# Performance work log

Hardware: AMD Instinct MI355X
Metric: run time of the kernel (lower is better)

Reference implementation:

```python
import jax, jax.numpy as jnp
import numpy as np
from jax import lax

C = 64   # channels
R = 2    # SKM expansion ratio
M = 4    # number of dilated convs
EPS = 1e-6


def conv3_dilated(x, w, b, d):
    # 3x3 conv, dilation d, padding d (same spatial size)
    y = lax.conv_general_dilated(x, w, (1, 1), [(d, d), (d, d)],
                                 rhs_dilation=(d, d),
                                 dimension_numbers=('NCHW', 'OIHW', 'NCHW'))
    return y + b[None, :, None, None]


def ln2d(x, g, b):
    # LayerNorm over channel dim at each spatial position (NAFNet LayerNorm2d)
    mu = x.mean(1, keepdims=True)
    var = x.var(1, keepdims=True)
    return (x - mu) / jnp.sqrt(var + EPS) * g[None, :, None, None] + b[None, :, None, None]


def skm(x, dw, db, c1w, c1b, pw):
    # dw: [M,C,C,3,3], db: [M,C], c1w: [R*C,C], c1b: [R*C], pw: [R*C, M*C]
    D = jnp.stack([conv3_dilated(x, dw[i], db[i], 2 * (i + 1)) for i in range(M)])  # [M,B,C,H,W]
    Z = D.sum(0).mean((-2, -1))                      # [B,C] global avg pool of summed branches
    S = jax.nn.relu(Z @ c1w.T + c1b)                 # [B,R*C]
    Sw = jax.nn.softmax((S @ pw).reshape(-1, M, C), axis=-1)  # [B,M,C], softmax over C
    return jnp.einsum('mbchw,bmc->bchw', D, Sw)      # weighted sum of branches


def setup_inputs() -> dict:
    key = jax.random.key(0)
    ks = jax.random.split(key, 24)
    B, H, W = 4, 96, 256
    sc = 0.05
    inp = {
        'x_l': jax.random.normal(ks[0], (B, C, H, W), jnp.float32),
        'x_r': jax.random.normal(ks[1], (B, C, H, W), jnp.float32),
        'lnl_g': jnp.ones((C,), jnp.float32),
        'lnl_b': jnp.zeros((C,), jnp.float32),
        'lnr_g': jnp.ones((C,), jnp.float32),
        'lnr_b': jnp.zeros((C,), jnp.float32),
        'l_dw': jax.random.normal(ks[2], (M, C, C, 3, 3), jnp.float32) * sc,
        'l_db': jax.random.normal(ks[3], (M, C), jnp.float32) * sc,
        'l_c1w': jax.random.normal(ks[4], (R * C, C), jnp.float32) * sc,
        'l_c1b': jax.random.normal(ks[5], (R * C,), jnp.float32) * sc,
        'l_pw': jax.random.normal(ks[6], (R * C, M * C), jnp.float32) * sc,
        'r_dw': jax.random.normal(ks[7], (M, C, C, 3, 3), jnp.float32) * sc,
        'r_db': jax.random.normal(ks[8], (M, C), jnp.float32) * sc,
        'r_c1w': jax.random.normal(ks[9], (R * C, C), jnp.float32) * sc,
        'r_c1b': jax.random.normal(ks[10], (R * C,), jnp.float32) * sc,
        'r_pw': jax.random.normal(ks[11], (R * C, M * C), jnp.float32) * sc,
        'l2w': jax.random.normal(ks[12], (C, C), jnp.float32) * sc,
        'l2b': jax.random.normal(ks[13], (C,), jnp.float32) * sc,
        'r2w': jax.random.normal(ks[14], (C, C), jnp.float32) * sc,
        'r2b': jax.random.normal(ks[15], (C,), jnp.float32) * sc,
        'beta': jax.random.normal(ks[16], (1, C, 1, 1), jnp.float32) * sc,
        'gamma': jax.random.normal(ks[17], (1, C, 1, 1), jnp.float32) * sc,
    }
    return inp


def reference(x_l, x_r, lnl_g, lnl_b, lnr_g, lnr_b,
              l_dw, l_db, l_c1w, l_c1b, l_pw,
              r_dw, r_db, r_c1w, r_c1b, r_pw,
              l2w, l2b, r2w, r2b, beta, gamma):
    scale = C ** (-0.5)
    Ql = skm(ln2d(x_l, lnl_g, lnl_b), l_dw, l_db, l_c1w, l_c1b, l_pw).transpose(0, 2, 3, 1)  # [B,H,W,C]
    Qr = skm(ln2d(x_r, lnr_g, lnr_b), r_dw, r_db, r_c1w, r_c1b, r_pw).transpose(0, 2, 3, 1)  # [B,H,W,C]
    Vl = (jnp.einsum('bchw,dc->bdhw', x_l, l2w) + l2b[None, :, None, None]).transpose(0, 2, 3, 1)
    Vr = (jnp.einsum('bchw,dc->bdhw', x_r, r2w) + r2b[None, :, None, None]).transpose(0, 2, 3, 1)
    attn = jnp.einsum('bhwc,bhvc->bhwv', Ql, Qr) * scale  # shared score matrix [B,H,W,W]
    F_r2l = jnp.einsum('bhwv,bhvc->bhwc', jax.nn.softmax(attn, axis=-1), Vr).transpose(0, 3, 1, 2)
    F_l2r = jnp.einsum('bhwv,bhwc->bhvc', jax.nn.softmax(attn, axis=-2), Vl).transpose(0, 3, 1, 2)
    return x_l + F_r2l * beta, x_r + F_l2r * gamma
```

## Files before the change

### kernel.cpp

```cpp
#include <hip/hip_runtime.h>
#include <hip/hip_bf16.h>
#include <cstdint>

constexpr int NB = 4;
constexpr int NC = 64;
constexpr int NH = 96;
constexpr int NW = 256;
constexpr int HWp = NH * NW;
constexpr float EPS = 1e-6f;

typedef __attribute__((ext_vector_type(8))) short short8;
typedef __attribute__((ext_vector_type(4))) short short4t;
typedef __attribute__((ext_vector_type(4))) float f32x4;

static __device__ __forceinline__ short f2bf(float f) {
    __hip_bfloat16 h = __float2bfloat16(f);
    return *reinterpret_cast<short*>(&h);
}

__global__ __launch_bounds__(256) void k_lnv(const float* __restrict__ x_l,
                                             const float* __restrict__ x_r,
                                             const float* __restrict__ gl,
                                             const float* __restrict__ bl,
                                             const float* __restrict__ gr,
                                             const float* __restrict__ br,
                                             short* __restrict__ XBl,
                                             short* __restrict__ XBr,
                                             float* __restrict__ R,
                                             const float* __restrict__ w2l,
                                             const float* __restrict__ b2l,
                                             const float* __restrict__ w2r,
                                             const float* __restrict__ b2r,
                                             short* __restrict__ VL,
                                             short* __restrict__ VR) {
    __shared__ float smem[8704];
    const int h = blockIdx.y, sideb = blockIdx.z;
    const int side = sideb >> 2, b = sideb & 3;
    const int t = threadIdx.x;

    if (blockIdx.x == 4) {
        const float* x = side ? x_r : x_l;
        const float* g = side ? gr : gl;
        const float* bta = side ? br : bl;
        short* XB = side ? XBr : XBl;
        float* xm = smem;

        const float* xp = x + ((size_t)b * NC * NH + h) * NW + t;
        float v[64];
        float s = 0.f, sq = 0.f;
#pragma unroll
        for (int c = 0; c < 64; ++c) {
            float tv = xp[(size_t)c * HWp];
            v[c] = tv; s += tv; sq += tv * tv;
        }
        float mu = s * (1.f / 64.f);
        float var = sq * (1.f / 64.f) - mu * mu;
        float rs = rsqrtf(var + EPS);
#pragma unroll
        for (int c = 0; c < 64; ++c) v[c] = (v[c] - mu) * rs * g[c] + bta[c];

#pragma unroll
        for (int chunk = 0; chunk < 4; ++chunk) {
            short8 s0, s1;
#pragma unroll
            for (int j = 0; j < 8; ++j) {
                s0[j] = f2bf(v[chunk * 16 + j]);
                s1[j] = f2bf(v[chunk * 16 + 8 + j]);
            }
            short* xb = XB + (((size_t)(b * 4 + chunk) * NH + h) * NW + t) * 16;
            *(short8*)xb = s0;
            *(short8*)(xb + 8) = s1;
        }

#pragma unroll
        for (int p = 0; p < 2; ++p) {
            const int cbase = p * 32;
            __syncthreads();
#pragma unroll
            for (int c = 0; c < 32; ++c)
                xm[c * 256 + (((t >> 2) ^ (c & 7)) << 2) + (t & 3)] = v[cbase + c];
            __syncthreads();
            const int cc = t & 31, q = t >> 5;
            float rsum = 0.f;
            float4 fs0 = {0,0,0,0}, fs1 = {0,0,0,0}, ls0 = {0,0,0,0}, ls1 = {0,0,0,0};
#pragma unroll
            for (int i = 0; i < 8; ++i) {
                int j4 = q * 8 + i;
                float4 f = *(const float4*)&xm[cc * 256 + ((j4 ^ (cc & 7)) << 2)];
                rsum += (f.x + f.y) + (f.z + f.w);
                if (i == 0) fs0 = f;
                if (i == 1) fs1 = f;
                if (i == 6) ls0 = f;
                if (i == 7) ls1 = f;
            }
            __syncthreads();
            xm[cc * 8 + q] = rsum;
            if (q == 7) {
                *(float4*)&xm[256 + cc * 8] = ls0;
                *(float4*)&xm[256 + cc * 8 + 4] = ls1;
            }
            __syncthreads();
            if (t < 32) {
                const int c = t;
                float full = 0.f;
#pragma unroll
                for (int q2 = 0; q2 < 8; ++q2) full += xm[c * 8 + q2];
                float h0 = xm[256 + c * 8 + 0], h1 = xm[256 + c * 8 + 1];
                float h2 = xm[256 + c * 8 + 2], h3 = xm[256 + c * 8 + 3];
                float h4 = xm[256 + c * 8 + 4], h5 = xm[256 + c * 8 + 5];
                float h6 = xm[256 + c * 8 + 6], h7 = xm[256 + c * 8 + 7];
                float e2 = fs0.x + fs0.y;
                float e4 = e2 + fs0.z + fs0.w;
                float e6 = e4 + fs1.x + fs1.y;
                float e8 = e6 + fs1.z + fs1.w;
                float r2 = h6 + h7;
                float r4 = (h4 + h5) + r2;
                float r6 = r4 + (h2 + h3);
                float r8 = r6 + (h0 + h1);
                float* Rp = R + ((size_t)(sideb * 64 + cbase + c) * NH + h) * 9;
                Rp[0] = full; Rp[1] = e2; Rp[2] = e4; Rp[3] = e6; Rp[4] = e8;
                Rp[5] = r2;  Rp[6] = r4; Rp[7] = r6; Rp[8] = r8;
            }
        }
    } else {
        const int wt = blockIdx.x;
        const float* x  = side ? x_r : x_l;
        const float* w2 = side ? w2r : w2l;
        const float* b2 = side ? b2r : b2l;
        short* VT = side ? VR : VL;
        const int lane = t & 63, q = t >> 6;
        float* xs  = smem;
        float* w2t = smem + 4352;
        int w0 = wt * 64;
        const float* src = x + (size_t)(b * 64) * HWp + h * NW + w0;
        for (int idx = t; idx < 4096; idx += 256) {
            int ci = idx >> 6, col = idx & 63;
            xs[ci * 68 + col] = src[(size_t)ci * HWp + col];
        }
        for (int idx = t; idx < 4096; idx += 256) {
            int co = idx >> 6, ci = idx & 63;
            w2t[ci * 68 + co] = w2[co * 64 + ci];
        }
        __syncthreads();

        const int pl0 = (lane & 15) * 4;
        const int c0 = q * 16 + (lane >> 4) * 4;
        f32x4 a4[4];
#pragma unroll
        for (int cc = 0; cc < 4; ++cc) {
            float bb = b2[c0 + cc];
            a4[cc] = (f32x4){bb, bb, bb, bb};
        }
        for (int ci = 0; ci < 64; ++ci) {
            f32x4 xv = *(const f32x4*)(xs + ci * 68 + pl0);
            f32x4 wv = *(const f32x4*)(w2t + ci * 68 + c0);
            a4[0] += xv * wv[0];
            a4[1] += xv * wv[1];
            a4[2] += xv * wv[2];
            a4[3] += xv * wv[3];
        }
        __syncthreads();
#pragma unroll
        for (int cc = 0; cc < 4; ++cc)
            *(f32x4*)(xs + (c0 + cc) * 68 + pl0) = a4[cc];
        __syncthreads();
        {
            int s = t & 63, g2 = t >> 6;
            int u = (s >> 2) + 16 * (s & 3);
#pragma unroll
            for (int cc = 0; cc < 16; ++cc) {
                int ch = g2 * 16 + cc;
                VT[((size_t)(b * 64 + ch) * NH + h) * NW + w0 + s] = f2bf(xs[ch * 68 + u]);
            }
        }
    }
}

__global__ __launch_bounds__(128) void k_comb(const float* __restrict__ R,
                                              float* __restrict__ T) {
    int x = blockIdx.x;
    int side = x >> 8, rem = x & 255, b = rem >> 6, ci = rem & 63;
    __shared__ float rp[NH][9];
    int t = threadIdx.x;
    const float* src = R + (size_t)x * NH * 9;
    for (int i = t; i < NH * 9; i += 128) ((float*)rp)[i] = src[i];
    __syncthreads();
    if (t < 36) {
        int m = t / 9, kh = (t % 9) / 3, kw = t % 3;
        int d = 2 * (m + 1);
        int r0 = (kh == 2) ? d : 0;
        int r1 = (kh == 0) ? NH - d : NH;
        float s = 0.f;
        for (int r = r0; r < r1; ++r) {
            float rowv = rp[r][0];
            if (kw == 0) rowv -= rp[r][5 + m];
            else if (kw == 2) rowv -= rp[r][1 + m];
            s += rowv;
        }
        T[side * 9216 + (b * 4 + m) * 576 + ci * 9 + kh * 3 + kw] = s;
    }
}

__global__ __launch_bounds__(256) void k_z(const float* __restrict__ T,
                                           const float* __restrict__ l_dw,
                                           const float* __restrict__ r_dw,
                                           const float* __restrict__ l_db,
                                           const float* __restrict__ r_db,
                                           float* __restrict__ Z) {
    int x = blockIdx.x;
    int side = x >> 8, bc = x & 255;
    int b = bc >> 6, c = bc & 63;
    const float* dw = side ? r_dw : l_dw;
    const float* db = side ? r_db : l_db;
    int t = threadIdx.x, lane = t & 63, m = t >> 6;
    const float* wp = dw + (size_t)(m * 64 + c) * 576;
    const float* tp = T + side * 9216 + (size_t)(b * 4 + m) * 576;
    float s = 0.f;
    for (int j = lane; j < 576; j += 64) s += wp[j] * tp[j];
#pragma unroll
    for (int o = 32; o; o >>= 1) s += __shfl_xor(s, o, 64);
    __shared__ float red[4];
    if (lane == 0) red[m] = s;
    __syncthreads();
    if (t == 0) {
        float z = (red[0] + red[1]) + (red[2] + red[3]);
        float bias = db[c] + db[64 + c] + db[128 + c] + db[192 + c];
        Z[x] = z * (1.f / (float)HWp) + bias;
    }
}

__global__ __launch_bounds__(256) void k_sel2(const float* __restrict__ Z,
                                              const float* __restrict__ l_db,
                                              const float* __restrict__ r_db,
                                              const float* __restrict__ l_c1w,
                                              const float* __restrict__ r_c1w,
                                              const float* __restrict__ l_c1b,
                                              const float* __restrict__ r_c1b,
                                              const float* __restrict__ l_pw,
                                              const float* __restrict__ r_pw,
                                              float* __restrict__ Sw,
                                              float* __restrict__ Qb) {
    int x = blockIdx.x;
    int side = x >> 2;
    const float* db  = side ? r_db  : l_db;
    const float* c1w = side ? r_c1w : l_c1w;
    const float* c1b = side ? r_c1b : l_c1b;
    const float* pw  = side ? r_pw  : l_pw;
    int t = threadIdx.x, lane = t & 63, wv = t >> 6;
    __shared__ float zs[64], ss[128], sw[256];
    __shared__ float cw[128 * 64];
    if (t < 64) zs[t] = Z[x * 64 + t];
    for (int i = t; i < 8192; i += 256) cw[i] = c1w[i];
    __syncthreads();
    if (t < 128) {
        float s = c1b[t];
        const float* wrow = cw + t * 64;
        for (int c = 0; c < 64; ++c) s += zs[c] * wrow[c];
        ss[t] = fmaxf(s, 0.f);
    }
    __syncthreads();
    float p = 0.f;
    for (int j = 0; j < 128; ++j) p += ss[j] * pw[j * 256 + t];
    float mx = p;
#pragma unroll
    for (int o = 32; o; o >>= 1) mx = fmaxf(mx, __shfl_xor(mx, o, 64));
    float e = __expf(p - mx);
    float sum = e;
#pragma unroll
    for (int o = 32; o; o >>= 1) sum += __shfl_xor(sum, o, 64);
    float swv = e / sum;
    Sw[(x * 4 + wv) * 64 + lane] = swv;
    sw[wv * 64 + lane] = swv;
    __syncthreads();
    if (t < 64) {
        float qb = sw[t] * db[t] + sw[64 + t] * db[64 + t]
                 + sw[128 + t] * db[128 + t] + sw[192 + t] * db[192 + t];
        Qb[x * 64 + t] = qb;
    }
}

__global__ __launch_bounds__(256) void k_fold(const float* __restrict__ l_dw,
                                              const float* __restrict__ r_dw,
                                              const float* __restrict__ Sw,
                                              short* __restrict__ WB) {
    int bx = blockIdx.x;
    int side = (bx >= 2304) ? 1 : 0;
    int idx = (bx - side * 2304) * 256 + threadIdx.x;
    const float* dw = side ? r_dw : l_dw;
    short* wbs = WB + (size_t)side * 589824;
    int kk = idx & 31;
    int co = (idx >> 5) & 63;
    int rest = idx >> 11;
    int tpair = rest % 18;
    int bc = rest / 18;
    int chunk = bc & 3, b = bc >> 2;
    int tpl = kk >> 4, cil = kk & 15;
    int tap = 2 * tpair + tpl;
    int m = tap / 9, k9 = tap % 9;
    int ci = chunk * 16 + cil;
    float val = Sw[((side * 4 + b) * 4 + m) * 64 + co]
              * dw[(size_t)((m * 64 + co) * 64 + ci) * 9 + k9];
    wbs[idx] = f2bf(val);
}

__global__ __launch_bounds__(256) void k_convm(const short* __restrict__ XBl,
                                               const short* __restrict__ XBr,
                                               const short* __restrict__ WBa,
                                               const float* __restrict__ QBa,
                                               short* __restrict__ QLs,
                                               short* __restrict__ QRs) {
    const int wt = blockIdx.x, h = blockIdx.y;
    const int side = blockIdx.z >> 2, b = blockIdx.z & 3;
    const short* XB = side ? XBr : XBl;
    const short* WB = WBa + (size_t)side * 589824;
    const float* Qb = QBa + side * 256;
    short* Qs = side ? QRs : QLs;
    const int t = threadIdx.x;
    const int lane = t & 63, wave = t >> 6;
    const int g = lane >> 4, ln15 = lane & 15;
    __shared__ short tile[2 * 9 * 144 * 8];

    f32x4 acc[8];
    {
        float qb = Qb[b * 64 + wave * 16 + ln15];
#pragma unroll
        for (int mt = 0; mt < 8; ++mt)
            acc[mt] = (f32x4){qb, qb, qb, qb};
    }
    const int w0 = wt * 128;
    const int halfoff = (g & 1) * (9 * 144 * 8);
    const int tsel = g >> 1;

    for (int chunk = 0; chunk < 4; ++chunk) {
        __syncthreads();
        const short* src = XB + (size_t)(b * 4 + chunk) * NH * NW * 16;
        for (int slot = t; slot < 9 * 144; slot += 256) {
            int r = slot / 144, col = slot % 144;
            int gh = h + 2 * r - 8;
            int gw = w0 - 8 + col;
            short8 v0 = {0, 0, 0, 0, 0, 0, 0, 0};
            short8 v1 = {0, 0, 0, 0, 0, 0, 0, 0};
            if (gh >= 0 && gh < NH && gw >= 0 && gw < NW) {
                const short* p = src + ((size_t)gh * NW + gw) * 16;
                v0 = *(const short8*)p;
                v1 = *(const short8*)(p + 8);
            }
            *(short8*)(tile + slot * 8) = v0;
            *(short8*)(tile + (9 * 144 + slot) * 8) = v1;
        }
        __syncthreads();

        const short* wbase = WB + (size_t)((b * 4 + chunk) * 18) * 2048
                           + wave * 512 + ln15 * 32 + g * 8;
#pragma unroll
        for (int tp = 0; tp < 18; ++tp) {
            const int ta = 2 * tp, tb = ta + 1;
            const int ma = ta / 9, k9a = ta % 9;
            const int mb = tb / 9, k9b = tb % 9;
            const int offA = ((4 + (ma + 1) * (k9a / 3 - 1)) * 144 + 8 + 2 * (ma + 1) * (k9a % 3 - 1)) * 8;
            const int offB = ((4 + (mb + 1) * (k9b / 3 - 1)) * 144 + 8 + 2 * (mb + 1) * (k9b % 3 - 1)) * 8;
            const int aoff = (tsel ? offB : offA) + ln15 * 8 + halfoff;
            short8 bf = *(const short8*)(wbase + (size_t)tp * 2048);
            const short* ap = tile + aoff;
            short8 a0 = *(const short8*)(ap);
            short8 a1 = *(const short8*)(ap + 128);
            short8 a2 = *(const short8*)(ap + 256);
            short8 a3 = *(const short8*)(ap + 384);
            short8 a4 = *(const short8*)(ap + 512);
            short8 a5 = *(const short8*)(ap + 640);
            short8 a6 = *(const short8*)(ap + 768);
            short8 a7 = *(const short8*)(ap + 896);
            acc[0] = __builtin_amdgcn_mfma_f32_16x16x32_bf16(a0, bf, acc[0], 0, 0, 0);
            acc[1] = __builtin_amdgcn_mfma_f32_16x16x32_bf16(a1, bf, acc[1], 0, 0, 0);
            acc[2] = __builtin_amdgcn_mfma_f32_16x16x32_bf16(a2, bf, acc[2], 0, 0, 0);
            acc[3] = __builtin_amdgcn_mfma_f32_16x16x32_bf16(a3, bf, acc[3], 0, 0, 0);
            acc[4] = __builtin_amdgcn_mfma_f32_16x16x32_bf16(a4, bf, acc[4], 0, 0, 0);
            acc[5] = __builtin_amdgcn_mfma_f32_16x16x32_bf16(a5, bf, acc[5], 0, 0, 0);
            acc[6] = __builtin_amdgcn_mfma_f32_16x16x32_bf16(a6, bf, acc[6], 0, 0, 0);
            acc[7] = __builtin_amdgcn_mfma_f32_16x16x32_bf16(a7, bf, acc[7], 0, 0, 0);
        }
    }
#pragma unroll
    for (int mt = 0; mt < 8; ++mt) {
        int px = w0 + mt * 16 + g * 4;
#pragma unroll
        for (int j = 0; j < 4; ++j) {
            Qs[((size_t)(b * NH + h) * NW + px + j) * 64 + wave * 16 + ln15]
                = f2bf(acc[mt][j]);
        }
    }
}

__global__ __launch_bounds__(128, 2) void k_attn(const short* __restrict__ QL,
                                                 const short* __restrict__ QR,
                                                 const short* __restrict__ VL,
                                                 const short* __restrict__ VR,
                                                 const float* __restrict__ x_l,
                                                 const float* __restrict__ x_r,
                                                 const float* __restrict__ beta,
                                                 const float* __restrict__ gamma,
                                                 float* __restrict__ out_all) {
    const int bx = blockIdx.x, h = blockIdx.y;
    const int side = blockIdx.z >> 2, b = blockIdx.z & 3;
    constexpr size_t PLANE = (size_t)NB * NC * NH * NW;
    const short* Qa  = side ? QR : QL;
    const short* Qbp = side ? QL : QR;
    const short* VT  = side ? VL : VR;
    const float* xres = side ? x_r : x_l;
    const float* scl  = side ? gamma : beta;
    float* out = out_all + (side ? PLANE : 0);

    const int t = threadIdx.x, lane = t & 63, wave = t >> 6;
    const int q = lane >> 4, c15 = lane & 15;
    __shared__ __align__(16) short PB[2][32 * 72];
    short* pb = PB[wave];

    const int wbase = bx * 64 + wave * 32;
    const short* qabase = Qa + ((size_t)(b * NH + h) * NW + wbase) * 64;
    const short* qbbase = Qbp + ((size_t)(b * NH + h) * NW) * 64;

    short8 afrag[2][2];
#pragma unroll
    for (int mt = 0; mt < 2; ++mt)
#pragma unroll
        for (int kk = 0; kk < 2; ++kk)
            afrag[mt][kk] = *(const short8*)(qabase + (mt * 16 + c15) * 64 + kk * 32 + q * 8);

    f32x4 osum[2][4];
#pragma unroll
    for (int mt = 0; mt < 2; ++mt)
#pragma unroll
        for (int nt = 0; nt < 4; ++nt) osum[mt][nt] = (f32x4){0.f, 0.f, 0.f, 0.f};
    float mrow[8], lrow[8];
#pragma unroll
    for (int i = 0; i < 8; ++i) { mrow[i] = -1e30f; lrow[i] = 0.f; }

    for (int vt = 0; vt < 4; ++vt) {
        f32x4 s[2][4];
#pragma unroll
        for (int mt = 0; mt < 2; ++mt)
#pragma unroll
            for (int nt = 0; nt < 4; ++nt) s[mt][nt] = (f32x4){0.f, 0.f, 0.f, 0.f};
#pragma unroll
        for (int kk = 0; kk < 2; ++kk) {
            short8 bq[4];
#pragma unroll
            for (int nt = 0; nt < 4; ++nt)
                bq[nt] = *(const short8*)(qbbase + (size_t)(vt * 64 + nt * 16 + c15) * 64 + kk * 32 + q * 8);
#pragma unroll
            for (int mt = 0; mt < 2; ++mt)
#pragma unroll
                for (int nt = 0; nt < 4; ++nt)
                    s[mt][nt] = __builtin_amdgcn_mfma_f32_16x16x32_bf16(afrag[mt][kk], bq[nt], s[mt][nt], 0, 0, 0);
        }
#pragma unroll
        for (int mt = 0; mt < 2; ++mt)
#pragma unroll
            for (int nt = 0; nt < 4; ++nt)
#pragma unroll
                for (int r = 0; r < 4; ++r) s[mt][nt][r] *= 0.125f;
        float al[8];
#pragma unroll
        for (int mt = 0; mt < 2; ++mt)
#pragma unroll
            for (int r = 0; r < 4; ++r) {
                float m0 = fmaxf(fmaxf(s[mt][0][r], s[mt][1][r]), fmaxf(s[mt][2][r], s[mt][3][r]));
#pragma unroll
                for (int msk = 1; msk < 16; msk <<= 1) m0 = fmaxf(m0, __shfl_xor(m0, msk, 64));
                int i = mt * 4 + r;
                float mn = fmaxf(mrow[i], m0);
                al[i] = __expf(mrow[i] - mn);
                mrow[i] = mn;
            }
#pragma unroll
        for (int mt = 0; mt < 2; ++mt)
#pragma unroll
            for (int r = 0; r < 4; ++r) {
                int i = mt * 4 + r;
                float m = mrow[i];
                float p0 = __expf(s[mt][0][r] - m);
                float p1 = __expf(s[mt][1][r] - m);
                float p2 = __expf(s[mt][2][r] - m);
                float p3 = __expf(s[mt][3][r] - m);
                short4t pk = {f2bf(p0), f2bf(p1), f2bf(p2), f2bf(p3)};
                *(short4t*)(pb + (mt * 16 + q * 4 + r) * 72 + c15 * 4) = pk;
                float lsv = (p0 + p1) + (p2 + p3);
#pragma unroll
                for (int msk = 1; msk < 16; msk <<= 1) lsv += __shfl_xor(lsv, msk, 64);
                lrow[i] = lrow[i] * al[i] + lsv;
            }
#pragma unroll
        for (int mt = 0; mt < 2; ++mt)
#pragma unroll
            for (int nt = 0; nt < 4; ++nt)
#pragma unroll
                for (int r = 0; r < 4; ++r) osum[mt][nt][r] *= al[mt * 4 + r];
#pragma unroll
        for (int kk = 0; kk < 2; ++kk) {
            short8 ap[2], bv[4];
#pragma unroll
            for (int mt = 0; mt < 2; ++mt)
                ap[mt] = *(const short8*)(pb + (mt * 16 + c15) * 72 + kk * 32 + q * 8);
#pragma unroll
            for (int nt = 0; nt < 4; ++nt)
                bv[nt] = *(const short8*)(VT + ((size_t)(b * 64 + nt * 16 + c15) * NH + h) * NW + vt * 64 + kk * 32 + q * 8);
#pragma unroll
            for (int mt = 0; mt < 2; ++mt)
#pragma unroll
                for (int nt = 0; nt < 4; ++nt)
                    osum[mt][nt] = __builtin_amdgcn_mfma_f32_16x16x32_bf16(ap[mt], bv[nt], osum[mt][nt], 0, 0, 0);
        }
    }
    float linv[8];
#pragma unroll
    for (int i = 0; i < 8; ++i) linv[i] = 1.f / lrow[i];
#pragma unroll
    for (int nt = 0; nt < 4; ++nt) {
        int c = nt * 16 + c15;
        float bv = scl[c];
        size_t pbase = ((size_t)(b * 64 + c) * NH + h) * NW + wbase;
#pragma unroll
        for (int mt = 0; mt < 2; ++mt)
#pragma unroll
            for (int r = 0; r < 4; ++r) {
                size_t o = pbase + mt * 16 + q * 4 + r;
                out[o] = xres[o] + osum[mt][nt][r] * linv[mt * 4 + r] * bv;
            }
    }
}

extern "C" void kernel_launch(void* const* d_in, const int* in_sizes, int n_in,
                              void* d_out, int out_size, void* d_ws, size_t ws_size,
                              hipStream_t stream) {
    const float* x_l   = (const float*)d_in[0];
    const float* x_r   = (const float*)d_in[1];
    const float* lnl_g = (const float*)d_in[2];
    const float* lnl_b = (const float*)d_in[3];
    const float* lnr_g = (const float*)d_in[4];
    const float* lnr_b = (const float*)d_in[5];
    const float* l_dw  = (const float*)d_in[6];
    const float* l_db  = (const float*)d_in[7];
    const float* l_c1w = (const float*)d_in[8];
    const float* l_c1b = (const float*)d_in[9];
    const float* l_pw  = (const float*)d_in[10];
    const float* r_dw  = (const float*)d_in[11];
    const float* r_db  = (const float*)d_in[12];
    const float* r_c1w = (const float*)d_in[13];
    const float* r_c1b = (const float*)d_in[14];
    const float* r_pw  = (const float*)d_in[15];
    const float* l2w   = (const float*)d_in[16];
    const float* l2b   = (const float*)d_in[17];
    const float* r2w   = (const float*)d_in[18];
    const float* r2b   = (const float*)d_in[19];
    const float* beta  = (const float*)d_in[20];
    const float* gamma = (const float*)d_in[21];
    float* out = (float*)d_out;

    constexpr size_t PLANE = (size_t)NB * NC * NH * NW;
    float* ws = (float*)d_ws;
    short* XBl = (short*)ws;         ws += PLANE / 2;
    short* XBr = (short*)ws;         ws += PLANE / 2;
    short* QLs = (short*)ws;         ws += PLANE / 2;
    short* QRs = (short*)ws;         ws += PLANE / 2;
    short* VLs = (short*)ws;         ws += PLANE / 2;
    short* VRs = (short*)ws;         ws += PLANE / 2;
    short* WB  = (short*)ws;         ws += 589824;
    float* Rb  = ws;                 ws += 442368;
    float* Tb  = ws;                 ws += 18432;
    float* SW  = ws;                 ws += 2048;
    float* QB  = ws;                 ws += 512;
    float* Zb  = ws;                 ws += 512;

    dim3 blk(256);
    k_lnv   <<<dim3(5, NH, 2 * NB), blk, 0, stream>>>(x_l, x_r, lnl_g, lnl_b, lnr_g, lnr_b,
                                                      XBl, XBr, Rb,
                                                      l2w, l2b, r2w, r2b, VLs, VRs);
    k_comb  <<<dim3(512), dim3(128), 0, stream>>>(Rb, Tb);
    k_z     <<<dim3(512), blk, 0, stream>>>(Tb, l_dw, r_dw, l_db, r_db, Zb);
    k_sel2  <<<dim3(8), blk, 0, stream>>>(Zb, l_db, r_db, l_c1w, r_c1w,
                                          l_c1b, r_c1b, l_pw, r_pw, SW, QB);
    k_fold  <<<dim3(4608), blk, 0, stream>>>(l_dw, r_dw, SW, WB);
    k_convm <<<dim3(2, NH, 2 * NB), blk, 0, stream>>>(XBl, XBr, WB, QB, QLs, QRs);
    k_attn  <<<dim3(4, NH, 2 * NB), dim3(128), 0, stream>>>(QLs, QRs, VLs, VRs,
                                                            x_l, x_r, beta, gamma, out);
}
```

Baseline: 315.5 us.

## Prefetch attention K/V fragments, remap blocks across XCDs, add MFMA priority

The attention kernel now loads the next key-tile fragments and the current V fragments into registers before the softmax step, so global loads overlap with exp/shuffle work instead of sitting directly before the MFMAs. It also uses a 1D grid remapped with a stride-8 interleave so consecutive blocks sharing the same row land on the same XCD for L2 reuse. s_setprio raises wave priority around the MFMA sections. The cost is higher register pressure, which could hurt the 2-blocks-per-CU occupancy target.

Result: no change. 321.8 us (+2.0%).

```diff
diff --git a/kernel.cpp b/kernel.cpp
--- a/kernel.cpp
+++ b/kernel.cpp
@@ -400,8 +400,13 @@
                                                  const float* __restrict__ beta,
                                                  const float* __restrict__ gamma,
                                                  float* __restrict__ out_all) {
-    const int bx = blockIdx.x, h = blockIdx.y;
-    const int side = blockIdx.z >> 2, b = blockIdx.z & 3;
+    const int p = blockIdx.x;
+    const int l = (p & 7) * 384 + (p >> 3);
+    const int bx = l & 3;
+    const int rest = l >> 2;
+    const int h = rest % 96;
+    const int zz = rest / 96;
+    const int side = zz >> 2, b = zz & 3;
     constexpr size_t PLANE = (size_t)NB * NC * NH * NW;
     const short* Qa  = side ? QR : QL;
     const short* Qbp = side ? QL : QR;
@@ -418,6 +423,7 @@
     const int wbase = bx * 64 + wave * 32;
     const short* qabase = Qa + ((size_t)(b * NH + h) * NW + wbase) * 64;
     const short* qbbase = Qbp + ((size_t)(b * NH + h) * NW) * 64;
+    const short* vbase  = VT + ((size_t)(b * 64 + c15) * NH + h) * NW;
 
     short8 afrag[2][2];
 #pragma unroll
@@ -435,24 +441,44 @@
 #pragma unroll
     for (int i = 0; i < 8; ++i) { mrow[i] = -1e30f; lrow[i] = 0.f; }
 
+    short8 bqc[2][4];
+#pragma unroll
+    for (int kk = 0; kk < 2; ++kk)
+#pragma unroll
+        for (int nt = 0; nt < 4; ++nt)
+            bqc[kk][nt] = *(const short8*)(qbbase + (size_t)(nt * 16 + c15) * 64 + kk * 32 + q * 8);
+
+#pragma unroll
     for (int vt = 0; vt < 4; ++vt) {
         f32x4 s[2][4];
 #pragma unroll
         for (int mt = 0; mt < 2; ++mt)
 #pragma unroll
             for (int nt = 0; nt < 4; ++nt) s[mt][nt] = (f32x4){0.f, 0.f, 0.f, 0.f};
-#pragma unroll
-        for (int kk = 0; kk < 2; ++kk) {
-            short8 bq[4];
+        __builtin_amdgcn_s_setprio(1);
+#pragma unroll
+        for (int kk = 0; kk < 2; ++kk)
+#pragma unroll
+            for (int mt = 0; mt < 2; ++mt)
+#pragma unroll
+                for (int nt = 0; nt < 4; ++nt)
+                    s[mt][nt] = __builtin_amdgcn_mfma_f32_16x16x32_bf16(afrag[mt][kk], bqc[kk][nt], s[mt][nt], 0, 0, 0);
+        __builtin_amdgcn_s_setprio(0);
+
+        short8 bvf[2][4];
+#pragma unroll
+        for (int kk = 0; kk < 2; ++kk)
 #pragma unroll
             for (int nt = 0; nt < 4; ++nt)
-                bq[nt] = *(const short8*)(qbbase + (size_t)(vt * 64 + nt * 16 + c15) * 64 + kk * 32 + q * 8);
-#pragma unroll
-            for (int mt = 0; mt < 2; ++mt)
+                bvf[kk][nt] = *(const short8*)(vbase + (size_t)(nt * 16) * NH * NW + vt * 64 + kk * 32 + q * 8);
+        if (vt < 3) {
+#pragma unroll
+            for (int kk = 0; kk < 2; ++kk)
 #pragma unroll
                 for (int nt = 0; nt < 4; ++nt)
-                    s[mt][nt] = __builtin_amdgcn_mfma_f32_16x16x32_bf16(afrag[mt][kk], bq[nt], s[mt][nt], 0, 0, 0);
-        }
+                    bqc[kk][nt] = *(const short8*)(qbbase + (size_t)((vt + 1) * 64 + nt * 16 + c15) * 64 + kk * 32 + q * 8);
+        }
+
 #pragma unroll
         for (int mt = 0; mt < 2; ++mt)
 #pragma unroll
@@ -495,21 +521,21 @@
             for (int nt = 0; nt < 4; ++nt)
 #pragma unroll
                 for (int r = 0; r < 4; ++r) osum[mt][nt][r] *= al[mt * 4 + r];
+
+        __builtin_amdgcn_s_setprio(1);
 #pragma unroll
         for (int kk = 0; kk < 2; ++kk) {
-            short8 ap[2], bv[4];
+            short8 ap[2];
 #pragma unroll
             for (int mt = 0; mt < 2; ++mt)
                 ap[mt] = *(const short8*)(pb + (mt * 16 + c15) * 72 + kk * 32 + q * 8);
 #pragma unroll
-            for (int nt = 0; nt < 4; ++nt)
-                bv[nt] = *(const short8*)(VT + ((size_t)(b * 64 + nt * 16 + c15) * NH + h) * NW + vt * 64 + kk * 32 + q * 8);
-#pragma unroll
             for (int mt = 0; mt < 2; ++mt)
 #pragma unroll
                 for (int nt = 0; nt < 4; ++nt)
-                    osum[mt][nt] = __builtin_amdgcn_mfma_f32_16x16x32_bf16(ap[mt], bv[nt], osum[mt][nt], 0, 0, 0);
-        }
+                    osum[mt][nt] = __builtin_amdgcn_mfma_f32_16x16x32_bf16(ap[mt], bvf[kk][nt], osum[mt][nt], 0, 0, 0);
+        }
+        __builtin_amdgcn_s_setprio(0);
     }
     float linv[8];
 #pragma unroll
@@ -517,14 +543,14 @@
 #pragma unroll
     for (int nt = 0; nt < 4; ++nt) {
         int c = nt * 16 + c15;
-        float bv = scl[c];
+        float scv = scl[c];
         size_t pbase = ((size_t)(b * 64 + c) * NH + h) * NW + wbase;
 #pragma unroll
         for (int mt = 0; mt < 2; ++mt)
 #pragma unroll
             for (int r = 0; r < 4; ++r) {
                 size_t o = pbase + mt * 16 + q * 4 + r;
-                out[o] = xres[o] + osum[mt][nt][r] * linv[mt * 4 + r] * bv;
+                out[o] = xres[o] + osum[mt][nt][r] * linv[mt * 4 + r] * scv;
             }
     }
 }
@@ -581,6 +607,6 @@
                                           l_c1b, r_c1b, l_pw, r_pw, SW, QB);
     k_fold  <<<dim3(4608), blk, 0, stream>>>(l_dw, r_dw, SW, WB);
     k_convm <<<dim3(2, NH, 2 * NB), blk, 0, stream>>>(XBl, XBr, WB, QB, QLs, QRs);
-    k_attn  <<<dim3(4, NH, 2 * NB), dim3(128), 0, stream>>>(QLs, QRs, VLs, VRs,
-                                                            x_l, x_r, beta, gamma, out);
-}
+    k_attn  <<<dim3(3072), dim3(128), 0, stream>>>(QLs, QRs, VLs, VRs,
+                                                   x_l, x_r, beta, gamma, out);
+}
```
